# Performance work log

Measured on AMD Instinct MI355X. Metric: run time of the kernel, lower is better.

The kernel has to match this reference:

```python
import jax, jax.numpy as jnp
import numpy as np

K = 8192
D = 512


def setup_inputs() -> dict:
    key = jax.random.key(0)
    k1, k2 = jax.random.split(key)
    x = jax.random.normal(k1, (64, 512, 512), dtype=jnp.float32)
    # nn.Embedding(K, D) with weight.uniform_(-1/K, 1/K)
    codebook = jax.random.uniform(k2, (K, D), dtype=jnp.float32,
                                  minval=-1.0 / K, maxval=1.0 / K)
    return {"x": x, "codebook": codebook}


def reference(x, codebook):
    # vq(x, codebook): nearest-neighbor codebook indices.
    d = codebook.shape[1]
    flat = x.reshape(-1, d)                              # [N, D]
    cb_sqr = jnp.sum(codebook * codebook, axis=1)        # [K]
    dists = cb_sqr[None, :] - 2.0 * jnp.einsum('nd,kd->nk', flat, codebook)  # [N, K]
    indices = jnp.argmin(dists, axis=1).astype(jnp.int32)
    return indices.reshape(x.shape[:-1])                 # latents = indices
```

## Files before the change

### kernel.cpp

```cpp
#include <hip/hip_runtime.h>


#define D_DIM 512
#define EPS_GAP 0.082f
#define KSPLIT 8

typedef __attribute__((ext_vector_type(4))) float f32x4;
typedef _Float16 half8v __attribute__((ext_vector_type(8)));
typedef _Float16 half4v __attribute__((ext_vector_type(4)));

__device__ __forceinline__ void gload_lds16(const void* g, void* l) {
    __builtin_amdgcn_global_load_lds(
        (const __attribute__((address_space(1))) unsigned int*)g,
        (__attribute__((address_space(3))) unsigned int*)l, 16, 0, 0);
}

__device__ __forceinline__ void ins3(float d, int i, float& d1, int& i1,
                                     float& d2, int& i2, float& d3) {
    if (d < d1 || (d == d1 && i < i1)) { d3 = d2; d2 = d1; i2 = i1; d1 = d; i1 = i; }
    else if (d < d2 || (d == d2 && i < i2)) { d3 = d2; d2 = d; i2 = i; }
    else if (d < d3) d3 = d;
}

__global__ __launch_bounds__(256) void prep_kernel(
        const float* __restrict__ X, const float* __restrict__ CB,
        _Float16* __restrict__ Xh, _Float16* __restrict__ Ch,
        float* __restrict__ cbs, int* __restrict__ cnt,
        int n4, int K, int cbBlocks, int xBlocks) {
    const int bid = blockIdx.x;
    const int tid = threadIdx.x;
    if (bid == 0 && tid == 0) *cnt = 0;
    if (bid < cbBlocks) {
        int w = bid * 4 + (tid >> 6);
        int lane = tid & 63;
        if (w >= K) return;
        size_t base = (size_t)w * D_DIM + lane * 8;
        const float4* r4 = (const float4*)(CB + base);
        float4 u = r4[0], v = r4[1];
        float s = u.x*u.x + u.y*u.y + u.z*u.z + u.w*u.w
                + v.x*v.x + v.y*v.y + v.z*v.z + v.w*v.w;
        half8v h;
        h[0] = (_Float16)(u.x * 4096.f); h[1] = (_Float16)(u.y * 4096.f);
        h[2] = (_Float16)(u.z * 4096.f); h[3] = (_Float16)(u.w * 4096.f);
        h[4] = (_Float16)(v.x * 4096.f); h[5] = (_Float16)(v.y * 4096.f);
        h[6] = (_Float16)(v.z * 4096.f); h[7] = (_Float16)(v.w * 4096.f);
        *(half8v*)(Ch + base) = h;
#pragma unroll
        for (int off = 32; off; off >>= 1) s += __shfl_xor(s, off);
        if (lane == 0) cbs[w] = s;
    } else {
        int i = (bid - cbBlocks) * 256 + tid;
        int stride = xBlocks * 256;
        for (; i < n4; i += stride) {
            float4 v = ((const float4*)X)[i];
            half4v h;
            h[0] = (_Float16)v.x; h[1] = (_Float16)v.y;
            h[2] = (_Float16)v.z; h[3] = (_Float16)v.w;
            ((half4v*)Xh)[i] = h;
        }
    }
}

__global__ __launch_bounds__(512, 2) void vq_mfma_kernel(
        const _Float16* __restrict__ Xh, const _Float16* __restrict__ Ch,
        const float* __restrict__ cbs,
        float* __restrict__ pd1, int* __restrict__ pi1,
        float* __restrict__ pd2, int* __restrict__ pi2,
        float* __restrict__ pd3, int N, int K) {

    __shared__ _Float16 As[3][256 * 64];
    __shared__ _Float16 Bs[3][128 * 64];
    __shared__ float cbsS[1024];

    const int tid  = threadIdx.x;
    const int lane = tid & 63;
    const int w    = tid >> 6;
    const int wr   = w >> 2;
    const int wcq  = w & 3;
    const int bid  = blockIdx.x;
    const int split     = bid & (KSPLIT - 1);
    const int rowBase   = (bid >> 3) * 128;
    const int kPerSplit = K / KSPLIT;
    const int splitBase = split * kPerSplit;
    const int NT        = kPerSplit / 256;
    const int nK        = NT * 8;

    for (int i = tid; i < kPerSplit; i += 512) cbsS[i] = cbs[splitBase + i];
    __syncthreads();

    const int tRow = tid >> 3;
    const int tColSw = (((tid & 7) ^ ((tid >> 3) & 1) ^ (((tid >> 4) & 1) << 2))) * 8;
    const int tDst = tid * 8;

    const int l15  = lane & 15;
    const int l4q  = lane >> 4;
    const int swl  = (l15 & 1) | (((l15 >> 1) & 1) << 2);
    const int aRowB = wr * 128 + l15;
    const int bRowB = wcq * 32 + l15;
    const int kOff0 = (l4q ^ swl) * 8;
    const int kOff1 = kOff0 ^ 32;

#define STAGE_AP(bufW_, kkT_, p_)                                             \
    do { int ct_ = (kkT_) >> 3, kt_ = (kkT_) & 7;                             \
        const _Float16* g_ = Ch + (size_t)(splitBase + ct_ * 256 +            \
                             (p_) * 128 + tRow) * D_DIM + kt_ * 64 + tColSw;  \
        gload_lds16(g_,               &As[bufW_][(p_) * 8192 + tDst]);        \
        gload_lds16(g_ + 64 * D_DIM,  &As[bufW_][(p_) * 8192 + 4096 + tDst]); \
    } while (0)
#define STAGE_B(bufW_, kkT_)                                                  \
    do { int kt_ = (kkT_) & 7;                                                \
        const _Float16* g_ = Xh + (size_t)(rowBase + tRow) * D_DIM            \
                             + kt_ * 64 + tColSw;                             \
        gload_lds16(g_,               &Bs[bufW_][tDst]);                      \
        gload_lds16(g_ + 64 * D_DIM,  &Bs[bufW_][4096 + tDst]);               \
    } while (0)

    float d1v[2], d2v[2], d3v[2];
    int   i1v[2], i2v[2];
#pragma unroll
    for (int nf = 0; nf < 2; ++nf) {
        d1v[nf] = 3.4e38f; d2v[nf] = 3.4e38f; d3v[nf] = 3.4e38f;
        i1v[nf] = 0x7fffffff; i2v[nf] = 0x7fffffff;
    }

    f32x4 acc[8][2];

    auto fold = [&](int ctF) {
        const int cb0 = ctF * 256 + wr * 128 + l4q * 4;
#pragma unroll
        for (int mf = 0; mf < 8; ++mf) {
            float4 c2q = *(const float4*)&cbsS[cb0 + mf * 16];
#pragma unroll
            for (int j = 0; j < 4; ++j) {
                const int code = splitBase + cb0 + mf * 16 + j;
                const float c2 = (&c2q.x)[j] * 4096.f;
#pragma unroll
                for (int nf = 0; nf < 2; ++nf) {
                    float dist = fmaf(-2.f, acc[mf][nf][j], c2);
                    ins3(dist, code, d1v[nf], i1v[nf], d2v[nf], i2v[nf], d3v[nf]);
                }
            }
        }
    };

    STAGE_AP(0, 0, 0); STAGE_AP(0, 0, 1); STAGE_B(0, 0);
    STAGE_AP(1, 1, 0); STAGE_AP(1, 1, 1); STAGE_B(1, 1);
    asm volatile("s_waitcnt vmcnt(6)" ::: "memory");
    __syncthreads();

    int bufR = 0;
    for (int kk = 0; kk < nK; ++kk) {
        const int bufW = (bufR >= 1) ? bufR - 1 : 2;
        const bool doS = (kk + 2) < nK;
        const _Float16* Ar = &As[bufR][0];
        const _Float16* Br = &Bs[bufR][0];

        if ((kk & 7) == 0) {
            if (kk) fold((kk >> 3) - 1);
#pragma unroll
            for (int mf = 0; mf < 8; ++mf)
#pragma unroll
                for (int nf = 0; nf < 2; ++nf)
#pragma unroll
                    for (int r = 0; r < 4; ++r) acc[mf][nf][r] = 0.f;
        }

        half8v bB[2][2];
#pragma unroll
        for (int nf = 0; nf < 2; ++nf) {
            bB[nf][0] = *(const half8v*)&Br[(bRowB + nf * 16) * 64 + kOff0];
            bB[nf][1] = *(const half8v*)&Br[(bRowB + nf * 16) * 64 + kOff1];
        }

#pragma unroll
        for (int q = 0; q < 4; ++q) {
            if (doS) {
                if (q == 0) STAGE_AP(bufW, kk + 2, 0);
                else if (q == 1) STAGE_AP(bufW, kk + 2, 1);
                else if (q == 2) STAGE_B(bufW, kk + 2);
            }
            half8v aA[2][2];
#pragma unroll
            for (int m = 0; m < 2; ++m) {
                aA[m][0] = *(const half8v*)&Ar[(aRowB + (2*q + m) * 16) * 64 + kOff0];
                aA[m][1] = *(const half8v*)&Ar[(aRowB + (2*q + m) * 16) * 64 + kOff1];
            }
            __builtin_amdgcn_s_setprio(1);
#pragma unroll
            for (int ksl = 0; ksl < 2; ++ksl)
#pragma unroll
                for (int m = 0; m < 2; ++m)
#pragma unroll
                    for (int nf = 0; nf < 2; ++nf)
                        acc[2*q + m][nf] = __builtin_amdgcn_mfma_f32_16x16x32_f16(
                            aA[m][ksl], bB[nf][ksl], acc[2*q + m][nf], 0, 0, 0);
            __builtin_amdgcn_s_setprio(0);
        }

        __builtin_amdgcn_sched_barrier(0);
        if (doS) asm volatile("s_waitcnt vmcnt(6)" ::: "memory");
        else     asm volatile("s_waitcnt vmcnt(0)" ::: "memory");
        __builtin_amdgcn_s_barrier();
        __builtin_amdgcn_sched_barrier(0);
        bufR = (bufR == 2) ? 0 : bufR + 1;
    }
    fold(NT - 1);

#pragma unroll
    for (int nf = 0; nf < 2; ++nf) {
#pragma unroll
        for (int off = 16; off <= 32; off <<= 1) {
            float od1 = __shfl_xor(d1v[nf], off);
            int   oi1 = __shfl_xor(i1v[nf], off);
            float od2 = __shfl_xor(d2v[nf], off);
            int   oi2 = __shfl_xor(i2v[nf], off);
            float od3 = __shfl_xor(d3v[nf], off);
            ins3(od1, oi1, d1v[nf], i1v[nf], d2v[nf], i2v[nf], d3v[nf]);
            ins3(od2, oi2, d1v[nf], i1v[nf], d2v[nf], i2v[nf], d3v[nf]);
            d3v[nf] = fminf(d3v[nf], od3);
        }
    }

    __syncthreads();
    float* mD1 = (float*)&As[0][0];
    int*   mI1 = (int*)(mD1 + 128);
    float* mD2 = (float*)(mD1 + 256);
    int*   mI2 = (int*)(mD1 + 384);
    float* mD3 = (float*)(mD1 + 512);
    if (wr == 1 && lane < 16) {
#pragma unroll
        for (int nf = 0; nf < 2; ++nf) {
            int x = wcq * 32 + nf * 16 + l15;
            mD1[x] = d1v[nf]; mI1[x] = i1v[nf];
            mD2[x] = d2v[nf]; mI2[x] = i2v[nf];
            mD3[x] = d3v[nf];
        }
    }
    __syncthreads();
    if (wr == 0 && lane < 16) {
#pragma unroll
        for (int nf = 0; nf < 2; ++nf) {
            int x = wcq * 32 + nf * 16 + l15;
            float d1 = d1v[nf], d2 = d2v[nf], d3 = d3v[nf];
            int i1 = i1v[nf], i2 = i2v[nf];
            ins3(mD1[x], mI1[x], d1, i1, d2, i2, d3);
            ins3(mD2[x], mI2[x], d1, i1, d2, i2, d3);
            d3 = fminf(d3, mD3[x]);
            size_t p = (size_t)split * N + (rowBase + x);
            pd1[p] = d1; pi1[p] = i1; pd2[p] = d2; pi2[p] = i2; pd3[p] = d3;
        }
    }
#undef STAGE_AP
#undef STAGE_B
}

__global__ __launch_bounds__(256) void combine_kernel(
        const float* __restrict__ X, const float* __restrict__ CB,
        const float* __restrict__ cbs,
        const float* __restrict__ pd1, const int* __restrict__ pi1,
        const float* __restrict__ pd2, const int* __restrict__ pi2,
        const float* __restrict__ pd3,
        int* __restrict__ out, int* __restrict__ flags, int* __restrict__ cnt,
        int N, int S) {
    const int row = blockIdx.x * 256 + threadIdx.x;
    if (row >= N) return;
    float d1 = pd1[row], d2 = pd2[row], d3 = pd3[row];
    int i1 = pi1[row], i2 = pi2[row];
    for (int s = 1; s < S; ++s) {
        size_t p = (size_t)s * N + row;
        ins3(pd1[p], pi1[p], d1, i1, d2, i2, d3);
        ins3(pd2[p], pi2[p], d1, i1, d2, i2, d3);
        d3 = fminf(d3, pd3[p]);
    }
    int best = i1;
    if (d2 - d1 < EPS_GAP) {
        if (d3 - d1 < EPS_GAP) {
            int f = atomicAdd(cnt, 1);
            flags[f] = row;
        } else {
            const float4* xr = (const float4*)(X + (size_t)row * D_DIM);
            const float4* ca = (const float4*)(CB + (size_t)i1 * D_DIM);
            const float4* cb = (const float4*)(CB + (size_t)i2 * D_DIM);
            float dotA = 0.f, dotB = 0.f;
#pragma unroll 4
            for (int d = 0; d < D_DIM / 4; ++d) {
                float4 xv = xr[d], av = ca[d], bv = cb[d];
                dotA = fmaf(xv.x, av.x, dotA); dotA = fmaf(xv.y, av.y, dotA);
                dotA = fmaf(xv.z, av.z, dotA); dotA = fmaf(xv.w, av.w, dotA);
                dotB = fmaf(xv.x, bv.x, dotB); dotB = fmaf(xv.y, bv.y, dotB);
                dotB = fmaf(xv.z, bv.z, dotB); dotB = fmaf(xv.w, bv.w, dotB);
            }
            float dA = fmaf(-2.f, dotA, cbs[i1]);
            float dB = fmaf(-2.f, dotB, cbs[i2]);
            best = (dB < dA || (dB == dA && i2 < i1)) ? i2 : i1;
        }
    }
    out[row] = best;
}

__global__ __launch_bounds__(256) void rare_scan_kernel(
        const float* __restrict__ X, const float* __restrict__ CB,
        const float* __restrict__ cbs,
        const int* __restrict__ flags, const int* __restrict__ cnt,
        float* __restrict__ scrD, int* __restrict__ scrI, int K) {
    __shared__ float xs[D_DIM];
    __shared__ float rD[4];
    __shared__ int   rI[4];
    const int nTasks = (*cnt) * 32;
    const int cpc = K / 32;
    for (int t = blockIdx.x; t < nTasks; t += gridDim.x) {
        const int fi = t >> 5, chunk = t & 31;
        const int row = flags[fi];
        __syncthreads();
        for (int i = threadIdx.x; i < D_DIM; i += 256)
            xs[i] = X[(size_t)row * D_DIM + i];
        __syncthreads();
        float bd = 3.4e38f; int bi = 0x7fffffff;
        for (int c = chunk * cpc + threadIdx.x; c < (chunk + 1) * cpc; c += 256) {
            const float4* cp = (const float4*)(CB + (size_t)c * D_DIM);
            float dot = 0.f;
#pragma unroll 4
            for (int d = 0; d < D_DIM / 4; ++d) {
                float4 cv = cp[d];
                float4 xv = *(const float4*)&xs[d * 4];
                dot = fmaf(xv.x, cv.x, dot); dot = fmaf(xv.y, cv.y, dot);
                dot = fmaf(xv.z, cv.z, dot); dot = fmaf(xv.w, cv.w, dot);
            }
            float dist = fmaf(-2.f, dot, cbs[c]);
            if (dist < bd || (dist == bd && c < bi)) { bd = dist; bi = c; }
        }
#pragma unroll
        for (int off = 1; off < 64; off <<= 1) {
            float od = __shfl_xor(bd, off);
            int   oi = __shfl_xor(bi, off);
            if (od < bd || (od == bd && oi < bi)) { bd = od; bi = oi; }
        }
        if ((threadIdx.x & 63) == 0) { rD[threadIdx.x >> 6] = bd; rI[threadIdx.x >> 6] = bi; }
        __syncthreads();
        if (threadIdx.x == 0) {
            for (int ww = 1; ww < 4; ++ww)
                if (rD[ww] < bd || (rD[ww] == bd && rI[ww] < bi)) {
                    bd = rD[ww]; bi = rI[ww];
                }
            scrD[t] = bd; scrI[t] = bi;
        }
    }
}

__global__ __launch_bounds__(256) void rare_write_kernel(
        const int* __restrict__ flags, const int* __restrict__ cnt,
        const float* __restrict__ scrD, const int* __restrict__ scrI,
        int* __restrict__ out) {
    const int nf = *cnt;
    for (int fi = blockIdx.x * 256 + threadIdx.x; fi < nf;
         fi += gridDim.x * 256) {
        float bd = scrD[fi * 32]; int bi = scrI[fi * 32];
        for (int ch = 1; ch < 32; ++ch) {
            float d = scrD[fi * 32 + ch]; int i = scrI[fi * 32 + ch];
            if (d < bd || (d == bd && i < bi)) { bd = d; bi = i; }
        }
        out[flags[fi]] = bi;
    }
}

#define BM 128
#define BN 128
#define BD 16

__global__ __launch_bounds__(256) void cbsqr_kernel(const float* __restrict__ cb,
                                                    float* __restrict__ out, int K) {
    int gtid = blockIdx.x * blockDim.x + threadIdx.x;
    int w = gtid >> 6;
    int lane = gtid & 63;
    if (w >= K) return;
    const float4* r4 = (const float4*)(cb + (size_t)w * D_DIM) + lane * 2;
    float4 u = r4[0], v = r4[1];
    float s = u.x*u.x + u.y*u.y + u.z*u.z + u.w*u.w
            + v.x*v.x + v.y*v.y + v.z*v.z + v.w*v.w;
#pragma unroll
    for (int off = 32; off; off >>= 1) s += __shfl_xor(s, off);
    if (lane == 0) out[w] = s;
}

__global__ __launch_bounds__(128) void vq_fp32_kernel(
        const float* __restrict__ X, const float* __restrict__ CB,
        const float* __restrict__ cbs,
        float* __restrict__ pd, int* __restrict__ pi,
        int* __restrict__ out, int N, int K, int nsplit) {

    __shared__ float As[BD][BM + 4];
    __shared__ float Bs[BD][BN + 4];

    const int tid = threadIdx.x;
    const int tx = tid & 7;
    const int ty = tid >> 3;
    const int rowBase = blockIdx.x * BM;
    const int split = blockIdx.y;
    const int kPer = K / nsplit;
    const int c0 = split * kPer, c1 = c0 + kPer;
    const int ldRow = tid >> 2;
    const int ldCol = (tid & 3) * 4;

    float bestD[8]; int bestI[8];
#pragma unroll
    for (int i = 0; i < 8; ++i) { bestD[i] = 3.4e38f; bestI[i] = 0; }

    for (int ct = c0; ct < c1; ct += BN) {
        float acc[8][16];
#pragma unroll
        for (int i = 0; i < 8; ++i)
#pragma unroll
            for (int j = 0; j < 16; ++j) acc[i][j] = 0.f;

        for (int dt = 0; dt < D_DIM; dt += BD) {
#pragma unroll
            for (int p = 0; p < 4; ++p) {
                int r = ldRow + p * 32;
                float4 av = *(const float4*)&X[(size_t)(rowBase + r) * D_DIM + dt + ldCol];
                float4 bv = *(const float4*)&CB[(size_t)(ct + r) * D_DIM + dt + ldCol];
                As[ldCol + 0][r] = av.x; As[ldCol + 1][r] = av.y;
                As[ldCol + 2][r] = av.z; As[ldCol + 3][r] = av.w;
                Bs[ldCol + 0][r] = bv.x; Bs[ldCol + 1][r] = bv.y;
                Bs[ldCol + 2][r] = bv.z; Bs[ldCol + 3][r] = bv.w;
            }
            __syncthreads();
#pragma unroll
            for (int d = 0; d < BD; ++d) {
                float4 a0 = *(const float4*)&As[d][ty * 4];
                float4 a1 = *(const float4*)&As[d][64 + ty * 4];
                float4 b0 = *(const float4*)&Bs[d][ 0 + tx * 4];
                float4 b1 = *(const float4*)&Bs[d][32 + tx * 4];
                float4 b2 = *(const float4*)&Bs[d][64 + tx * 4];
                float4 b3 = *(const float4*)&Bs[d][96 + tx * 4];
                float a[8] = {a0.x,a0.y,a0.z,a0.w,a1.x,a1.y,a1.z,a1.w};
                float b[16] = {b0.x,b0.y,b0.z,b0.w, b1.x,b1.y,b1.z,b1.w,
                               b2.x,b2.y,b2.z,b2.w, b3.x,b3.y,b3.z,b3.w};
#pragma unroll
                for (int i = 0; i < 8; ++i)
#pragma unroll
                    for (int j = 0; j < 16; ++j)
                        acc[i][j] = fmaf(a[i], b[j], acc[i][j]);
            }
            __syncthreads();
        }
#pragma unroll
        for (int j = 0; j < 16; ++j) {
            int code = ct + (j >> 2) * 32 + tx * 4 + (j & 3);
            float c2v = cbs[code];
#pragma unroll
            for (int i = 0; i < 8; ++i) {
                float dist = fmaf(-2.f, acc[i][j], c2v);
                if (dist < bestD[i]) { bestD[i] = dist; bestI[i] = code; }
            }
        }
    }
#pragma unroll
    for (int i = 0; i < 8; ++i) {
        float bd = bestD[i]; int bi = bestI[i];
#pragma unroll
        for (int off = 1; off < 8; off <<= 1) {
            float od = __shfl_xor(bd, off);
            int   oi = __shfl_xor(bi, off);
            if (od < bd || (od == bd && oi < bi)) { bd = od; bi = oi; }
        }
        if (tx == 0) {
            int row = rowBase + ((i < 4) ? ty * 4 + i : 64 + ty * 4 + (i - 4));
            if (nsplit == 1) out[row] = bi;
            else {
                pd[(size_t)row * nsplit + split] = bd;
                pi[(size_t)row * nsplit + split] = bi;
            }
        }
    }
}

__global__ __launch_bounds__(256) void combine_fp32_kernel(
        const float* __restrict__ pd, const int* __restrict__ pi,
        int* __restrict__ out, int N, int S) {
    int r = blockIdx.x * blockDim.x + threadIdx.x;
    if (r >= N) return;
    float bd = pd[(size_t)r * S];
    int bi = pi[(size_t)r * S];
    for (int s = 1; s < S; ++s) {
        float d = pd[(size_t)r * S + s];
        int i = pi[(size_t)r * S + s];
        if (d < bd || (d == bd && i < bi)) { bd = d; bi = i; }
    }
    out[r] = bi;
}

extern "C" void kernel_launch(void* const* d_in, const int* in_sizes, int n_in,
                              void* d_out, int out_size, void* d_ws, size_t ws_size,
                              hipStream_t stream) {
    const float* X  = (const float*)d_in[0];
    const float* CB = (const float*)d_in[1];
    const int N = in_sizes[0] / D_DIM;
    const int K = in_sizes[1] / D_DIM;
    int* out = (int*)d_out;

    size_t o = 0;
    auto take = [&](size_t bytes) { size_t r = o; o += (bytes + 255) & ~(size_t)255; return r; };
    size_t oCbs = take((size_t)K * 4);
    size_t oXh  = take((size_t)N * D_DIM * 2);
    size_t oCh  = take((size_t)K * D_DIM * 2);
    size_t oPd1 = take((size_t)N * KSPLIT * 4);
    size_t oPi1 = take((size_t)N * KSPLIT * 4);
    size_t oPd2 = take((size_t)N * KSPLIT * 4);
    size_t oPi2 = take((size_t)N * KSPLIT * 4);
    size_t oPd3 = take((size_t)N * KSPLIT * 4);
    size_t oFlg = take((size_t)N * 4);
    size_t oCnt = take(256);
    size_t oScD = take((size_t)N * 32 * 4);
    size_t oScI = take((size_t)N * 32 * 4);
    const size_t need = o;

    char* ws = (char*)d_ws;
    float* cbs = (float*)(ws + oCbs);

    if (ws_size >= need && (N % 128) == 0 && (K % (KSPLIT * 256)) == 0 &&
        (K / KSPLIT) <= 1024 && (K % 32) == 0) {
        _Float16* Xh = (_Float16*)(ws + oXh);
        _Float16* Ch = (_Float16*)(ws + oCh);
        float* pd1 = (float*)(ws + oPd1);
        int*   pi1 = (int*)(ws + oPi1);
        float* pd2 = (float*)(ws + oPd2);
        int*   pi2 = (int*)(ws + oPi2);
        float* pd3 = (float*)(ws + oPd3);
        int* flags = (int*)(ws + oFlg);
        int* cnt   = (int*)(ws + oCnt);
        float* scrD = (float*)(ws + oScD);
        int*   scrI = (int*)(ws + oScI);

        const int cbBlocks = K / 4;
        const int xBlocks  = 2048;
        prep_kernel<<<cbBlocks + xBlocks, 256, 0, stream>>>(
            X, CB, Xh, Ch, cbs, cnt, N * D_DIM / 4, K, cbBlocks, xBlocks);

        vq_mfma_kernel<<<(N / 128) * KSPLIT, 512, 0, stream>>>(
            Xh, Ch, cbs, pd1, pi1, pd2, pi2, pd3, N, K);

        combine_kernel<<<N / 256, 256, 0, stream>>>(
            X, CB, cbs, pd1, pi1, pd2, pi2, pd3, out, flags, cnt, N, KSPLIT);

        rare_scan_kernel<<<1024, 256, 0, stream>>>(
            X, CB, cbs, flags, cnt, scrD, scrI, K);

        rare_write_kernel<<<32, 256, 0, stream>>>(flags, cnt, scrD, scrI, out);
    } else {
        size_t base = ((size_t)K * 4 + 255) & ~(size_t)255;
        int nsplit = 4;
        while (nsplit > 1 &&
               (ws_size < base + (size_t)N * nsplit * 8 || (K % (nsplit * BN)) != 0))
            nsplit >>= 1;
        float* pd = (float*)(ws + base);
        int*   pi = (int*)(ws + base + (size_t)N * nsplit * 4);
        cbsqr_kernel<<<(K + 3) / 4, 256, 0, stream>>>(CB, cbs, K);
        dim3 grid(N / BM, nsplit);
        vq_fp32_kernel<<<grid, 128, 0, stream>>>(X, CB, cbs, pd, pi, out, N, K, nsplit);
        if (nsplit > 1)
            combine_fp32_kernel<<<(N + 255) / 256, 256, 0, stream>>>(pd, pi, out, N, nsplit);
    }
}
```

Measured before the change: 596.6 us.

## Spread top-3 fold across next tile's K iterations using a copied accumulator

Instead of folding all 8 accumulator fragments into the top-3 candidates in one burst at each tile boundary, the accumulators are copied to a second register set and one fragment is folded per K-step of the following tile. The aim is to interleave the scalar compare/insert work with MFMA issue so the matrix pipe is not idle during the fold. The cost is 64 extra accumulator registers per thread, which risks lower occupancy or spills, and fold_piece uses a runtime index kt into accP, which may force scratch or indexing overhead.

```diff
diff --git a/kernel.cpp b/kernel.cpp
--- a/kernel.cpp
+++ b/kernel.cpp
@@ -123,9 +123,23 @@
         i1v[nf] = 0x7fffffff; i2v[nf] = 0x7fffffff;
     }
 
-    f32x4 acc[8][2];
-
-    auto fold = [&](int ctF) {
+    f32x4 acc[8][2], accP[8][2];
+
+    auto fold_piece = [&](int ctF, int mf) {
+        const int cb0 = ctF * 256 + wr * 128 + l4q * 4 + mf * 16;
+        float4 c2q = *(const float4*)&cbsS[cb0];
+#pragma unroll
+        for (int j = 0; j < 4; ++j) {
+            const int code = splitBase + cb0 + j;
+            const float c2 = (&c2q.x)[j] * 4096.f;
+#pragma unroll
+            for (int nf = 0; nf < 2; ++nf) {
+                float dist = fmaf(-2.f, accP[mf][nf][j], c2);
+                ins3(dist, code, d1v[nf], i1v[nf], d2v[nf], i2v[nf], d3v[nf]);
+            }
+        }
+    };
+    auto fold_acc = [&](int ctF) {
         const int cb0 = ctF * 256 + wr * 128 + l4q * 4;
 #pragma unroll
         for (int mf = 0; mf < 8; ++mf) {
@@ -152,17 +166,20 @@
     for (int kk = 0; kk < nK; ++kk) {
         const int bufW = (bufR >= 1) ? bufR - 1 : 2;
         const bool doS = (kk + 2) < nK;
+        const int kt = kk & 7;
         const _Float16* Ar = &As[bufR][0];
         const _Float16* Br = &Bs[bufR][0];
 
-        if ((kk & 7) == 0) {
-            if (kk) fold((kk >> 3) - 1);
+        if (kt == 0) {
 #pragma unroll
             for (int mf = 0; mf < 8; ++mf)
 #pragma unroll
                 for (int nf = 0; nf < 2; ++nf)
 #pragma unroll
-                    for (int r = 0; r < 4; ++r) acc[mf][nf][r] = 0.f;
+                    for (int r = 0; r < 4; ++r) {
+                        accP[mf][nf][r] = acc[mf][nf][r];
+                        acc[mf][nf][r] = 0.f;
+                    }
         }
 
         half8v bB[2][2];
@@ -196,6 +213,8 @@
                             aA[m][ksl], bB[nf][ksl], acc[2*q + m][nf], 0, 0, 0);
             __builtin_amdgcn_s_setprio(0);
         }
+
+        if (kk >= 8) fold_piece((kk >> 3) - 1, kt);
 
         __builtin_amdgcn_sched_barrier(0);
         if (doS) asm volatile("s_waitcnt vmcnt(6)" ::: "memory");
@@ -204,7 +223,7 @@
         __builtin_amdgcn_sched_barrier(0);
         bufR = (bufR == 2) ? 0 : bufR + 1;
     }
-    fold(NT - 1);
+    fold_acc(NT - 1);
 
 #pragma unroll
     for (int nf = 0; nf < 2; ++nf) {
```

Result: slower. 854.0 us (+43.1%).
